# Kernel tuning notes

Hardware: AMD Instinct MI355X
Metric: run time of the kernel (lower is better)

## Reference

```python
import jax, jax.numpy as jnp
import numpy as np

N_NODES = 50000
N_EDGES = 800000
N_GRAPHS = 256
HIDDEN = 128
N_LAYERS = 5
OUT_DIM = 10
BN_EPS = 1e-5


def _batchnorm(z, gamma, beta):
    # training-mode BatchNorm1d over node axis, biased variance (as torch)
    m = z.mean(axis=0)
    v = z.var(axis=0)
    return (z - m) * jax.lax.rsqrt(v + BN_EPS) * gamma + beta


def setup_inputs() -> dict:
    key = jax.random.key(0)
    ks = jax.random.split(key, 16)
    s = 0.05
    x = jax.random.normal(ks[0], (N_NODES, HIDDEN), dtype=jnp.float32)
    edge_index = jax.random.randint(ks[1], (2, N_EDGES), 0, N_NODES, dtype=jnp.int32)
    batch = jnp.sort(jax.random.randint(ks[2], (N_NODES,), 0, N_GRAPHS, dtype=jnp.int32))
    return {
        "x": x,
        "conv_W1": jax.random.normal(ks[3], (N_LAYERS, HIDDEN, HIDDEN), dtype=jnp.float32) * s,
        "conv_b1": jnp.zeros((N_LAYERS, HIDDEN), jnp.float32),
        "mlp_bn_g": jnp.ones((N_LAYERS, HIDDEN), jnp.float32),
        "mlp_bn_b": jnp.zeros((N_LAYERS, HIDDEN), jnp.float32),
        "conv_W2": jax.random.normal(ks[4], (N_LAYERS, HIDDEN, HIDDEN), dtype=jnp.float32) * s,
        "conv_b2": jnp.zeros((N_LAYERS, HIDDEN), jnp.float32),
        "out_bn_g": jnp.ones((N_LAYERS, HIDDEN), jnp.float32),
        "out_bn_b": jnp.zeros((N_LAYERS, HIDDEN), jnp.float32),
        "fc1_W": jax.random.normal(ks[5], (HIDDEN * N_LAYERS, HIDDEN), dtype=jnp.float32) * s,
        "fc1_b": jnp.zeros((HIDDEN,), jnp.float32),
        "fc2_W": jax.random.normal(ks[6], (HIDDEN, OUT_DIM), dtype=jnp.float32) * s,
        "fc2_b": jnp.zeros((OUT_DIM,), jnp.float32),
        "edge_index": edge_index,
        "batch": batch,
    }


def reference(x, conv_W1, conv_b1, mlp_bn_g, mlp_bn_b, conv_W2, conv_b2,
              out_bn_g, out_bn_b, fc1_W, fc1_b, fc2_W, fc2_b,
              edge_index, batch):
    src, dst = edge_index[0], edge_index[1]
    h = x
    pooled = []
    for i in range(N_LAYERS):
        # GINConv, eps=0: mlp(h + sum_{j in N(v)} h_j)
        agg = jax.ops.segment_sum(h[src], dst, num_segments=N_NODES)
        z = h + agg
        z = z @ conv_W1[i] + conv_b1[i]
        z = jax.nn.relu(_batchnorm(z, mlp_bn_g[i], mlp_bn_b[i]))
        z = z @ conv_W2[i] + conv_b2[i]
        # outer BN + ReLU (self.bns)
        h = jax.nn.relu(_batchnorm(z, out_bn_g[i], out_bn_b[i]))
        pooled.append(jax.ops.segment_sum(h, batch, num_segments=N_GRAPHS))
    out = jnp.concatenate(pooled, axis=-1)          # [G, L*hidden]
    out = jax.nn.relu(out @ fc1_W + fc1_b)
    # dropout in eval mode -> identity
    out = out @ fc2_W + fc2_b                       # [G, out_dim]
    return out
```

## Files before the change

### kernel.cpp

```cpp
#include <hip/hip_runtime.h>

#define N_NODES 50000
#define N_EDGES 800000
#define N_GRAPHS 256
#define HIDDEN 128
#define N_LAYERS 5
#define OUT_DIM 10
#define BN_EPS 1e-5f

#define BUCKET_SHIFT 7
#define BUCKET_NODES 128
#define N_BUCKETS ((N_NODES + BUCKET_NODES - 1) / BUCKET_NODES)
#define STAGE_THREADS 1024
#define STAGE_EPB 4096

typedef __bf16 bf16x8 __attribute__((ext_vector_type(8)));
typedef float f32x4 __attribute__((ext_vector_type(4)));

union FragAB {
    bf16x8 v;
    ushort s[8];
    uint4 q;
};

__device__ inline float bf2f(ushort u) {
    union { uint i; float f; } v;
    v.i = ((uint)u) << 16;
    return v.f;
}

__device__ inline float bf2f_lo(uint u) {
    union { uint i; float f; } v;
    v.i = u << 16;
    return v.f;
}

__device__ inline float bf2f_hi(uint u) {
    union { uint i; float f; } v;
    v.i = u & 0xffff0000u;
    return v.f;
}

__device__ inline ushort f2bf(float f) {
    union { float f; uint u; } v;
    v.f = f;
    uint b = v.u;
    uint r = (b + 0x7fffu + ((b >> 16) & 1u)) >> 16;
    return (ushort)r;
}


__global__ void k_hist(const int* __restrict__ dst, int* __restrict__ counts) {
    int e = blockIdx.x * blockDim.x + threadIdx.x;
    if (e < N_EDGES) atomicAdd(&counts[dst[e]], 1);
}

__global__ void k_scan_blocks(const int* __restrict__ in, int* __restrict__ out,
                              int* __restrict__ bsum, int n) {
    __shared__ int s[256];
    int i = blockIdx.x * 256 + threadIdx.x;
    int v = (i < n) ? in[i] : 0;
    s[threadIdx.x] = v;
    __syncthreads();
    for (int off = 1; off < 256; off <<= 1) {
        int t = (threadIdx.x >= off) ? s[threadIdx.x - off] : 0;
        __syncthreads();
        s[threadIdx.x] += t;
        __syncthreads();
    }
    if (i < n) out[i] = s[threadIdx.x];
    if (threadIdx.x == 255) bsum[blockIdx.x] = s[255];
}

__global__ void k_scan_sums(int* __restrict__ bsum, int nb) {
    __shared__ int s[256];
    int t = threadIdx.x;
    int v = (t < nb) ? bsum[t] : 0;
    s[t] = v;
    __syncthreads();
    for (int off = 1; off < 256; off <<= 1) {
        int tv = (t >= off) ? s[t - off] : 0;
        __syncthreads();
        s[t] += tv;
        __syncthreads();
    }
    int excl = (t == 0) ? 0 : s[t - 1];
    if (t < nb) bsum[t] = excl;
}

__global__ void k_offsets(const int* __restrict__ scanned, const int* __restrict__ boff,
                          int* __restrict__ offsets, int* __restrict__ bcur, int n) {
    int i = blockIdx.x * 256 + threadIdx.x;
    if (i < n) {
        int val = scanned[i] + boff[blockIdx.x];
        offsets[i + 1] = val;
        if (((i + 1) & (BUCKET_NODES - 1)) == 0 && (i + 1) < n)
            bcur[(i + 1) >> BUCKET_SHIFT] = val;
    }
    if (i == 0) {
        offsets[0] = 0;
        bcur[0] = 0;
    }
}

__global__ __launch_bounds__(STAGE_THREADS) void k_stage(const int* __restrict__ esrc,
                                                         const int* __restrict__ edst,
                                                         int* __restrict__ bcur,
                                                         uint* __restrict__ stage) {
    __shared__ int lcnt[N_BUCKETS];
    __shared__ int lbase[N_BUCKETS];
    int tid = threadIdx.x;
    for (int i = tid; i < N_BUCKETS; i += STAGE_THREADS) lcnt[i] = 0;
    __syncthreads();
    int e0 = blockIdx.x * STAGE_EPB;
    uint pk[4];
    int bk[4];
    bool val[4];
#pragma unroll
    for (int i = 0; i < 4; ++i) {
        int e = e0 + i * STAGE_THREADS + tid;
        val[i] = e < N_EDGES;
        bk[i] = 0;
        pk[i] = 0;
        if (val[i]) {
            int d = edst[e];
            int s = esrc[e];
            bk[i] = d >> BUCKET_SHIFT;
            pk[i] = (uint)s | ((uint)(d & (BUCKET_NODES - 1)) << 16);
            atomicAdd(&lcnt[bk[i]], 1);
        }
    }
    __syncthreads();
    for (int i = tid; i < N_BUCKETS; i += STAGE_THREADS) {
        int c = lcnt[i];
        lbase[i] = c ? atomicAdd(&bcur[i], c) : 0;
        lcnt[i] = 0;
    }
    __syncthreads();
#pragma unroll
    for (int i = 0; i < 4; ++i) {
        if (val[i]) {
            int off = atomicAdd(&lcnt[bk[i]], 1);
            stage[lbase[bk[i]] + off] = pk[i];
        }
    }
}

__global__ __launch_bounds__(256) void k_fill2(const uint* __restrict__ stage,
                                               const int* __restrict__ offsets,
                                               ushort* __restrict__ adj) {
    __shared__ int lcur[BUCKET_NODES];
    int bk = blockIdx.x;
    int n0 = bk * BUCKET_NODES;
    int n1 = n0 + BUCKET_NODES;
    if (n1 > N_NODES) n1 = N_NODES;
    int cnt = n1 - n0;
    if ((int)threadIdx.x < cnt) lcur[threadIdx.x] = offsets[n0 + threadIdx.x];
    __syncthreads();
    int s = offsets[n0];
    int e = offsets[n1];
    for (int i = s + threadIdx.x; i < e; i += 256) {
        uint pk = stage[i];
        int dl = pk >> 16;
        int pos = atomicAdd(&lcur[dl], 1);
        adj[pos] = (ushort)(pk & 0xffffu);
    }
}


#define CVT_BLKS 6250

__global__ __launch_bounds__(256) void k_prep(const float* __restrict__ x,
                                              ushort* __restrict__ xb,
                                              const float* __restrict__ W1,
                                              const float* __restrict__ W2,
                                              ushort* __restrict__ Wp) {
    if (blockIdx.x < CVT_BLKS) {
        int i = blockIdx.x * 256 + threadIdx.x;
        float4 v = ((const float4*)x)[i];
        ushort4 o;
        o.x = f2bf(v.x); o.y = f2bf(v.y); o.z = f2bf(v.z); o.w = f2bf(v.w);
        ((ushort4*)xb)[i] = o;
    } else {
        int mat = blockIdx.x - CVT_BLKS;
        const float* src = (mat < 5) ? (W1 + (size_t)mat * 16384)
                                     : (W2 + (size_t)(mat - 5) * 16384);
        ushort* dst = Wp + (size_t)mat * 16384;
        for (int idx = threadIdx.x; idx < 16384; idx += 256) {
            int jj = idx & 7;
            int frag = idx >> 3;
            int lane = frag & 63;
            int cf = frag >> 6;
            int ct = cf >> 2, kc = cf & 3;
            int k = kc * 32 + (lane >> 4) * 8 + jj;
            int c = (lane & 15) * 8 + ct;
            dst[idx] = f2bf(src[k * 128 + c]);
        }
    }
}


__global__ __launch_bounds__(256) void k_agg(const ushort* __restrict__ h,
                                             const int* __restrict__ offsets,
                                             const ushort* __restrict__ adj,
                                             ushort* __restrict__ y) {
    int wave = threadIdx.x >> 6;
    int lane = threadIdx.x & 63;
    int e = lane >> 4, c16 = lane & 15;
    int v = blockIdx.x * 4 + wave;
    const uint4* h4 = (const uint4*)h;

    int off = offsets[v];
    int end = offsets[v + 1];

    float a0 = 0.f, a1 = 0.f, a2 = 0.f, a3 = 0.f;
    float a4 = 0.f, a5 = 0.f, a6 = 0.f, a7 = 0.f;

#define ACC8(T)                                      \
    {                                                \
        a0 += bf2f_lo(T.x); a1 += bf2f_hi(T.x);      \
        a2 += bf2f_lo(T.y); a3 += bf2f_hi(T.y);      \
        a4 += bf2f_lo(T.z); a5 += bf2f_hi(T.z);      \
        a6 += bf2f_lo(T.w); a7 += bf2f_hi(T.w);      \
    }

    int u[8];
    bool val[8];
#pragma unroll
    for (int k = 0; k < 8; ++k) {
        int idx = off + k * 4 + e;
        val[k] = idx < end;
        u[k] = adj[val[k] ? idx : 0];
    }
    uint4 t[8];
#pragma unroll
    for (int k = 0; k < 8; ++k)
        t[k] = h4[(size_t)u[k] * 16 + c16];
#pragma unroll
    for (int k = 0; k < 8; ++k) {
        if (val[k]) ACC8(t[k])
    }

    for (int j = off + 32; j < end; j += 4) {
        bool valid = (j + e) < end;
        int uu = adj[valid ? (j + e) : 0];
        uint4 tt = h4[(size_t)uu * 16 + c16];
        if (valid) ACC8(tt)
    }

    a0 += __shfl_xor(a0, 16, 64); a0 += __shfl_xor(a0, 32, 64);
    a1 += __shfl_xor(a1, 16, 64); a1 += __shfl_xor(a1, 32, 64);
    a2 += __shfl_xor(a2, 16, 64); a2 += __shfl_xor(a2, 32, 64);
    a3 += __shfl_xor(a3, 16, 64); a3 += __shfl_xor(a3, 32, 64);
    a4 += __shfl_xor(a4, 16, 64); a4 += __shfl_xor(a4, 32, 64);
    a5 += __shfl_xor(a5, 16, 64); a5 += __shfl_xor(a5, 32, 64);
    a6 += __shfl_xor(a6, 16, 64); a6 += __shfl_xor(a6, 32, 64);
    a7 += __shfl_xor(a7, 16, 64); a7 += __shfl_xor(a7, 32, 64);
    if (e == 0) {
        uint4 self = h4[(size_t)v * 16 + c16];
        ACC8(self)
        uint4 pk;
        pk.x = (uint)f2bf(a0) | ((uint)f2bf(a1) << 16);
        pk.y = (uint)f2bf(a2) | ((uint)f2bf(a3) << 16);
        pk.z = (uint)f2bf(a4) | ((uint)f2bf(a5) << 16);
        pk.w = (uint)f2bf(a6) | ((uint)f2bf(a7) << 16);
        ((uint4*)y)[(size_t)v * 16 + c16] = pk;
    }
#undef ACC8
}


template <bool ACT>
__global__ __launch_bounds__(256) void k_gemm(const ushort* __restrict__ A,
                                              const ushort* __restrict__ Wp,
                                              const float* __restrict__ bias,
                                              const float* __restrict__ g,
                                              const float* __restrict__ b,
                                              const float* __restrict__ statIn,
                                              ushort* __restrict__ Z,
                                              float* __restrict__ statOut) {
    __shared__ float scs[128];
    __shared__ float shs[128];
    __shared__ float redS[4][128];
    __shared__ float redQ[4][128];

    int tid = threadIdx.x;
    int w = tid >> 6, lane = tid & 63;
    int m = lane & 15, quad = lane >> 4;
    int r0 = blockIdx.x * 64;

    if (ACT) {
        if (tid < 128) {
            float s = 0.f, q = 0.f;
#pragma unroll
            for (int sl = 0; sl < 8; ++sl) {
                s += statIn[sl * 256 + tid];
                q += statIn[sl * 256 + 128 + tid];
            }
            float mn = s * (1.f / N_NODES);
            float var = q * (1.f / N_NODES) - mn * mn;
            float sc = g[tid] * rsqrtf(var + BN_EPS);
            scs[tid] = sc;
            shs[tid] = b[tid] - mn * sc;
        }
        __syncthreads();
    }

    int arow = r0 + w * 16 + m;
    if (arow >= N_NODES) arow = N_NODES - 1;

    f32x4 acc[8];
#pragma unroll
    for (int ct = 0; ct < 8; ++ct) acc[ct] = (f32x4){0.f, 0.f, 0.f, 0.f};

    const uint4* Wp4 = (const uint4*)Wp;

#pragma unroll
    for (int kc = 0; kc < 4; ++kc) {
        FragAB a;
        a.q = *(const uint4*)(A + (size_t)arow * 128 + kc * 32 + quad * 8);
        if (ACT) {
            int k0 = kc * 32 + quad * 8;
#pragma unroll
            for (int jj = 0; jj < 8; ++jj) {
                float fv = bf2f(a.s[jj]);
                fv = fmaxf(fv * scs[k0 + jj] + shs[k0 + jj], 0.f);
                a.s[jj] = f2bf(fv);
            }
        }
#pragma unroll
        for (int ct = 0; ct < 8; ++ct) {
            FragAB bf;
            bf.q = Wp4[(ct * 4 + kc) * 64 + lane];
            acc[ct] = __builtin_amdgcn_mfma_f32_16x16x32_bf16(a.v, bf.v, acc[ct], 0, 0, 0);
        }
    }

    int rbase = r0 + w * 16 + quad * 4;
    float bc[8];
#pragma unroll
    for (int ct = 0; ct < 8; ++ct) bc[ct] = bias[m * 8 + ct];

    float st[8], sq[8];
#pragma unroll
    for (int ct = 0; ct < 8; ++ct) { st[ct] = 0.f; sq[ct] = 0.f; }

#pragma unroll
    for (int i = 0; i < 4; ++i) {
        int row = rbase + i;
        if (row < N_NODES) {
            float v[8];
#pragma unroll
            for (int ct = 0; ct < 8; ++ct) {
                v[ct] = acc[ct][i] + bc[ct];
                st[ct] += v[ct];
                sq[ct] += v[ct] * v[ct];
            }
            uint4 pk;
            pk.x = (uint)f2bf(v[0]) | ((uint)f2bf(v[1]) << 16);
            pk.y = (uint)f2bf(v[2]) | ((uint)f2bf(v[3]) << 16);
            pk.z = (uint)f2bf(v[4]) | ((uint)f2bf(v[5]) << 16);
            pk.w = (uint)f2bf(v[6]) | ((uint)f2bf(v[7]) << 16);
            *(uint4*)(Z + (size_t)row * 128 + m * 8) = pk;
        }
    }
#pragma unroll
    for (int ct = 0; ct < 8; ++ct) {
        st[ct] += __shfl_xor(st[ct], 16, 64);
        st[ct] += __shfl_xor(st[ct], 32, 64);
        sq[ct] += __shfl_xor(sq[ct], 16, 64);
        sq[ct] += __shfl_xor(sq[ct], 32, 64);
    }
    if (quad == 0) {
#pragma unroll
        for (int ct = 0; ct < 8; ++ct) {
            redS[w][m * 8 + ct] = st[ct];
            redQ[w][m * 8 + ct] = sq[ct];
        }
    }
    __syncthreads();
    if (tid < 128) {
        float s = redS[0][tid] + redS[1][tid] + redS[2][tid] + redS[3][tid];
        float q = redQ[0][tid] + redQ[1][tid] + redQ[2][tid] + redQ[3][tid];
        int slot = (blockIdx.x & 7) * 256;
        atomicAdd(&statOut[slot + tid], s);
        atomicAdd(&statOut[slot + 128 + tid], q);
    }
}


__global__ __launch_bounds__(256) void k_apply_pool(const ushort* __restrict__ z2,
                                                    const float* __restrict__ statIn,
                                                    const float* __restrict__ g,
                                                    const float* __restrict__ b,
                                                    const int* __restrict__ batch,
                                                    ushort* __restrict__ h,
                                                    float* __restrict__ pooled) {
    int w = threadIdx.x >> 6, lane = threadIdx.x & 63;
    int c0 = lane * 2;
    float s0 = 0.f, q0 = 0.f, s1 = 0.f, q1 = 0.f;
#pragma unroll
    for (int sl = 0; sl < 8; ++sl) {
        s0 += statIn[sl * 256 + c0];
        q0 += statIn[sl * 256 + 128 + c0];
        s1 += statIn[sl * 256 + c0 + 1];
        q1 += statIn[sl * 256 + 128 + c0 + 1];
    }
    float mn0 = s0 * (1.f / N_NODES);
    float var0 = q0 * (1.f / N_NODES) - mn0 * mn0;
    float sc0 = g[c0] * rsqrtf(var0 + BN_EPS);
    float sh0 = b[c0] - mn0 * sc0;
    float mn1 = s1 * (1.f / N_NODES);
    float var1 = q1 * (1.f / N_NODES) - mn1 * mn1;
    float sc1 = g[c0 + 1] * rsqrtf(var1 + BN_EPS);
    float sh1 = b[c0 + 1] - mn1 * sc1;

    int r0 = blockIdx.x * 256 + w * 64;
    int r1 = r0 + 64;
    if (r1 > N_NODES) r1 = N_NODES;
    if (r0 >= N_NODES) return;

    int bidx = r0 + lane;
    int myb = batch[bidx < N_NODES ? bidx : (N_NODES - 1)];

    float a0 = 0.f, a1 = 0.f;
    int curg = -1;
    const uint* z1 = (const uint*)z2;
    uint* h1 = (uint*)h;
    for (int r = r0; r < r1; ++r) {
        uint t = z1[(size_t)r * 64 + lane];
        float v0 = fmaxf(bf2f((ushort)(t & 0xffff)) * sc0 + sh0, 0.f);
        float v1 = fmaxf(bf2f((ushort)(t >> 16)) * sc1 + sh1, 0.f);
        h1[(size_t)r * 64 + lane] = (uint)f2bf(v0) | ((uint)f2bf(v1) << 16);
        int gg = __shfl(myb, r - r0, 64);
        if (gg != curg) {
            if (curg >= 0) {
                atomicAdd(&pooled[(size_t)curg * 640 + c0], a0);
                atomicAdd(&pooled[(size_t)curg * 640 + c0 + 1], a1);
            }
            a0 = 0.f; a1 = 0.f;
            curg = gg;
        }
        a0 += v0;
        a1 += v1;
    }
    if (curg >= 0) {
        atomicAdd(&pooled[(size_t)curg * 640 + c0], a0);
        atomicAdd(&pooled[(size_t)curg * 640 + c0 + 1], a1);
    }
}


__global__ __launch_bounds__(128) void k_mlp(const float* __restrict__ pooled,
                                             const float* __restrict__ fc1W,
                                             const float* __restrict__ fc1b,
                                             const float* __restrict__ fc2W,
                                             const float* __restrict__ fc2b,
                                             float* __restrict__ out) {
    __shared__ float p[640];
    __shared__ float hid[128];
    int g = blockIdx.x;
    int t = threadIdx.x;
    for (int i = t; i < 640; i += 128) p[i] = pooled[(size_t)g * 640 + i];
    __syncthreads();
    float a = fc1b[t];
    for (int k = 0; k < 640; ++k) a += p[k] * fc1W[(size_t)k * 128 + t];
    hid[t] = fmaxf(a, 0.f);
    __syncthreads();
    if (t < OUT_DIM) {
        float o = fc2b[t];
#pragma unroll 8
        for (int c = 0; c < 128; ++c) o += hid[c] * fc2W[(size_t)c * OUT_DIM + t];
        out[(size_t)g * OUT_DIM + t] = o;
    }
}


static inline char* align256(char* p) {
    return (char*)(((uintptr_t)p + 255) & ~(uintptr_t)255);
}

extern "C" void kernel_launch(void* const* d_in, const int* in_sizes, int n_in,
                              void* d_out, int out_size, void* d_ws, size_t ws_size,
                              hipStream_t stream) {
    const float* x    = (const float*)d_in[0];
    const float* W1   = (const float*)d_in[1];
    const float* b1   = (const float*)d_in[2];
    const float* bng1 = (const float*)d_in[3];
    const float* bnb1 = (const float*)d_in[4];
    const float* W2   = (const float*)d_in[5];
    const float* b2   = (const float*)d_in[6];
    const float* bng2 = (const float*)d_in[7];
    const float* bnb2 = (const float*)d_in[8];
    const float* fc1W = (const float*)d_in[9];
    const float* fc1b = (const float*)d_in[10];
    const float* fc2W = (const float*)d_in[11];
    const float* fc2b = (const float*)d_in[12];
    const int* ei     = (const int*)d_in[13];
    const int* batch  = (const int*)d_in[14];
    const int* esrc = ei;
    const int* edst = ei + N_EDGES;

    const size_t NF = (size_t)N_NODES * HIDDEN;
    char* p = (char*)d_ws;
    ushort* ybf  = (ushort*)p; p = align256(p + NF * 2);
    ushort* z1bf = (ushort*)p; p = align256(p + NF * 2);
    ushort* hbf  = (ushort*)p; p = align256(p + NF * 2);
    ushort* xbf  = (ushort*)p; p = align256(p + NF * 2);
    ushort* Wp   = (ushort*)p; p = align256(p + (size_t)10 * 16384 * 2);
    float* pooled = (float*)p; p += (size_t)N_GRAPHS * 640 * 4;
    float* stats  = (float*)p; p = align256(p + (size_t)10 * 8 * 256 * 4);
    int* counts   = (int*)p; p = align256(p + (size_t)N_NODES * 4);
    int* offsets  = (int*)p; p = align256(p + (size_t)(N_NODES + 1) * 4);
    int* bcur     = (int*)p; p = align256(p + (size_t)N_BUCKETS * 4);
    int* bsum     = (int*)p; p = align256(p + 256 * 4);
    ushort* adj   = (ushort*)p; p = align256(p + (size_t)N_EDGES * 2);
    uint* stage   = (uint*)p; p = align256(p + (size_t)N_EDGES * 4);

    hipMemsetAsync(counts, 0, (size_t)N_NODES * 4, stream);
    hipMemsetAsync(pooled, 0, ((size_t)N_GRAPHS * 640 + (size_t)10 * 8 * 256) * 4, stream);

    const int SCAN_BLKS = (N_NODES + 255) / 256;
    k_hist<<<(N_EDGES + 255) / 256, 256, 0, stream>>>(edst, counts);
    {
        int* scanscratch = (int*)stage;
        k_scan_blocks<<<SCAN_BLKS, 256, 0, stream>>>(counts, scanscratch, bsum, N_NODES);
        k_scan_sums<<<1, 256, 0, stream>>>(bsum, SCAN_BLKS);
        k_offsets<<<SCAN_BLKS, 256, 0, stream>>>(scanscratch, bsum, offsets, bcur, N_NODES);
    }
    k_stage<<<(N_EDGES + STAGE_EPB - 1) / STAGE_EPB, STAGE_THREADS, 0, stream>>>(esrc, edst, bcur, stage);
    k_fill2<<<N_BUCKETS, 256, 0, stream>>>(stage, offsets, adj);

    k_prep<<<CVT_BLKS + 10, 256, 0, stream>>>(x, xbf, W1, W2, Wp);

    const int GEMM_BLKS = (N_NODES + 63) / 64;
    const int POOL_BLKS = (N_NODES + 255) / 256;
    for (int l = 0; l < N_LAYERS; ++l) {
        const ushort* hin = (l == 0) ? xbf : hbf;
        float* st1 = stats + (size_t)(2 * l) * 2048;
        float* st2 = stats + (size_t)(2 * l + 1) * 2048;

        k_agg<<<N_NODES / 4, 256, 0, stream>>>(hin, offsets, adj, ybf);

        k_gemm<false><<<GEMM_BLKS, 256, 0, stream>>>(
            ybf, Wp + (size_t)l * 16384, b1 + l * 128,
            nullptr, nullptr, nullptr, z1bf, st1);

        k_gemm<true><<<GEMM_BLKS, 256, 0, stream>>>(
            z1bf, Wp + (size_t)(5 + l) * 16384, b2 + l * 128,
            bng1 + l * 128, bnb1 + l * 128, st1, ybf, st2);

        k_apply_pool<<<POOL_BLKS, 256, 0, stream>>>(
            ybf, st2, bng2 + l * 128, bnb2 + l * 128, batch, hbf, pooled + l * 128);
    }

    k_mlp<<<N_GRAPHS, 128, 0, stream>>>(pooled, fc1W, fc1b, fc2W, fc2b, (float*)d_out);
}
```

Baseline: 568.3 us.

## Fuse outer BN+ReLU into next layer's aggregation and merge pooling launch

Drops the materialized h tensor. The outer BatchNorm+ReLU is now applied on the fly to z2 inside the next layer's neighbor gather, and that kernel also runs the graph pooling in separate blocks of the same launch. This removes a full write of h per layer and one kernel launch per layer. In exchange the BN affine+ReLU is recomputed for every gathered edge (about 16x per node), adding ALU work to the gather path and some register pressure.

```diff
diff --git a/kernel.cpp b/kernel.cpp
--- a/kernel.cpp
+++ b/kernel.cpp
@@ -13,6 +13,8 @@
 #define N_BUCKETS ((N_NODES + BUCKET_NODES - 1) / BUCKET_NODES)
 #define STAGE_THREADS 1024
 #define STAGE_EPB 4096
+#define POOL_BLKS ((N_NODES + 255) / 256)
+#define AGG_BLKS (N_NODES / 4)
 
 typedef __bf16 bf16x8 __attribute__((ext_vector_type(8)));
 typedef float f32x4 __attribute__((ext_vector_type(4)));
@@ -200,29 +202,38 @@
 }
 
 
-__global__ __launch_bounds__(256) void k_agg(const ushort* __restrict__ h,
-                                             const int* __restrict__ offsets,
-                                             const ushort* __restrict__ adj,
-                                             ushort* __restrict__ y) {
-    int wave = threadIdx.x >> 6;
-    int lane = threadIdx.x & 63;
-    int e = lane >> 4, c16 = lane & 15;
-    int v = blockIdx.x * 4 + wave;
-    const uint4* h4 = (const uint4*)h;
-
+#define ACC8_BN(T)                                                  \
+    {                                                               \
+        float f0 = bf2f_lo(T.x), f1 = bf2f_hi(T.x);                 \
+        float f2 = bf2f_lo(T.y), f3 = bf2f_hi(T.y);                 \
+        float f4 = bf2f_lo(T.z), f5 = bf2f_hi(T.z);                 \
+        float f6 = bf2f_lo(T.w), f7 = bf2f_hi(T.w);                 \
+        if (BN) {                                                   \
+            f0 = fmaxf(f0 * sc[0] + sh[0], 0.f);                    \
+            f1 = fmaxf(f1 * sc[1] + sh[1], 0.f);                    \
+            f2 = fmaxf(f2 * sc[2] + sh[2], 0.f);                    \
+            f3 = fmaxf(f3 * sc[3] + sh[3], 0.f);                    \
+            f4 = fmaxf(f4 * sc[4] + sh[4], 0.f);                    \
+            f5 = fmaxf(f5 * sc[5] + sh[5], 0.f);                    \
+            f6 = fmaxf(f6 * sc[6] + sh[6], 0.f);                    \
+            f7 = fmaxf(f7 * sc[7] + sh[7], 0.f);                    \
+        }                                                           \
+        a0 += f0; a1 += f1; a2 += f2; a3 += f3;                     \
+        a4 += f4; a5 += f5; a6 += f6; a7 += f7;                     \
+    }
+
+template <bool BN>
+__device__ inline void agg_one_node(int v, const uint4* __restrict__ h4,
+                                    const int* __restrict__ offsets,
+                                    const ushort* __restrict__ adj,
+                                    ushort* __restrict__ y,
+                                    int e, int c16,
+                                    const float* sc, const float* sh) {
     int off = offsets[v];
     int end = offsets[v + 1];
 
     float a0 = 0.f, a1 = 0.f, a2 = 0.f, a3 = 0.f;
     float a4 = 0.f, a5 = 0.f, a6 = 0.f, a7 = 0.f;
-
-#define ACC8(T)                                      \
-    {                                                \
-        a0 += bf2f_lo(T.x); a1 += bf2f_hi(T.x);      \
-        a2 += bf2f_lo(T.y); a3 += bf2f_hi(T.y);      \
-        a4 += bf2f_lo(T.z); a5 += bf2f_hi(T.z);      \
-        a6 += bf2f_lo(T.w); a7 += bf2f_hi(T.w);      \
-    }
 
     int u[8];
     bool val[8];
@@ -238,14 +249,13 @@
         t[k] = h4[(size_t)u[k] * 16 + c16];
 #pragma unroll
     for (int k = 0; k < 8; ++k) {
-        if (val[k]) ACC8(t[k])
-    }
-
+        if (val[k]) ACC8_BN(t[k])
+    }
     for (int j = off + 32; j < end; j += 4) {
         bool valid = (j + e) < end;
         int uu = adj[valid ? (j + e) : 0];
         uint4 tt = h4[(size_t)uu * 16 + c16];
-        if (valid) ACC8(tt)
+        if (valid) ACC8_BN(tt)
     }
 
     a0 += __shfl_xor(a0, 16, 64); a0 += __shfl_xor(a0, 32, 64);
@@ -258,7 +268,7 @@
     a7 += __shfl_xor(a7, 16, 64); a7 += __shfl_xor(a7, 32, 64);
     if (e == 0) {
         uint4 self = h4[(size_t)v * 16 + c16];
-        ACC8(self)
+        ACC8_BN(self)
         uint4 pk;
         pk.x = (uint)f2bf(a0) | ((uint)f2bf(a1) << 16);
         pk.y = (uint)f2bf(a2) | ((uint)f2bf(a3) << 16);
@@ -266,7 +276,168 @@
         pk.w = (uint)f2bf(a6) | ((uint)f2bf(a7) << 16);
         ((uint4*)y)[(size_t)v * 16 + c16] = pk;
     }
-#undef ACC8
+}
+
+__global__ __launch_bounds__(256) void k_agg_first(const ushort* __restrict__ h,
+                                                   const int* __restrict__ offsets,
+                                                   const ushort* __restrict__ adj,
+                                                   ushort* __restrict__ y) {
+    int wave = threadIdx.x >> 6;
+    int lane = threadIdx.x & 63;
+    int v = blockIdx.x * 4 + wave;
+    agg_one_node<false>(v, (const uint4*)h, offsets, adj, y,
+                        lane >> 4, lane & 15, nullptr, nullptr);
+}
+
+__global__ __launch_bounds__(256) void k_aggpool(const ushort* __restrict__ z2,
+                                                 const float* __restrict__ statIn,
+                                                 const float* __restrict__ g,
+                                                 const float* __restrict__ b,
+                                                 const int* __restrict__ batch,
+                                                 float* __restrict__ pooled,
+                                                 const int* __restrict__ offsets,
+                                                 const ushort* __restrict__ adj,
+                                                 ushort* __restrict__ y) {
+    int tid = threadIdx.x;
+    int w = tid >> 6, lane = tid & 63;
+
+    if (blockIdx.x >= POOL_BLKS) {
+        __shared__ float scs[128];
+        __shared__ float shs[128];
+        if (tid < 128) {
+            float s = 0.f, q = 0.f;
+#pragma unroll
+            for (int sl = 0; sl < 8; ++sl) {
+                s += statIn[sl * 256 + tid];
+                q += statIn[sl * 256 + 128 + tid];
+            }
+            float mn = s * (1.f / N_NODES);
+            float var = q * (1.f / N_NODES) - mn * mn;
+            float scv = g[tid] * rsqrtf(var + BN_EPS);
+            scs[tid] = scv;
+            shs[tid] = b[tid] - mn * scv;
+        }
+        __syncthreads();
+        int c16 = lane & 15;
+        float sc[8], sh[8];
+#pragma unroll
+        for (int j = 0; j < 8; ++j) {
+            sc[j] = scs[c16 * 8 + j];
+            sh[j] = shs[c16 * 8 + j];
+        }
+        int v = (blockIdx.x - POOL_BLKS) * 4 + w;
+        agg_one_node<true>(v, (const uint4*)z2, offsets, adj, y,
+                           lane >> 4, c16, sc, sh);
+        return;
+    }
+
+    int c0 = lane * 2;
+    float s0 = 0.f, q0 = 0.f, s1 = 0.f, q1 = 0.f;
+#pragma unroll
+    for (int sl = 0; sl < 8; ++sl) {
+        s0 += statIn[sl * 256 + c0];
+        q0 += statIn[sl * 256 + 128 + c0];
+        s1 += statIn[sl * 256 + c0 + 1];
+        q1 += statIn[sl * 256 + 128 + c0 + 1];
+    }
+    float mn0 = s0 * (1.f / N_NODES);
+    float var0 = q0 * (1.f / N_NODES) - mn0 * mn0;
+    float sc0 = g[c0] * rsqrtf(var0 + BN_EPS);
+    float sh0 = b[c0] - mn0 * sc0;
+    float mn1 = s1 * (1.f / N_NODES);
+    float var1 = q1 * (1.f / N_NODES) - mn1 * mn1;
+    float sc1 = g[c0 + 1] * rsqrtf(var1 + BN_EPS);
+    float sh1 = b[c0 + 1] - mn1 * sc1;
+
+    int r0 = blockIdx.x * 256 + w * 64;
+    int r1 = r0 + 64;
+    if (r1 > N_NODES) r1 = N_NODES;
+    if (r0 >= N_NODES) return;
+
+    int bidx = r0 + lane;
+    int myb = batch[bidx < N_NODES ? bidx : (N_NODES - 1)];
+
+    float a0 = 0.f, a1 = 0.f;
+    int curg = -1;
+    const uint* z1 = (const uint*)z2;
+    for (int r = r0; r < r1; ++r) {
+        uint t = z1[(size_t)r * 64 + lane];
+        float v0 = fmaxf(bf2f((ushort)(t & 0xffff)) * sc0 + sh0, 0.f);
+        float v1 = fmaxf(bf2f((ushort)(t >> 16)) * sc1 + sh1, 0.f);
+        int gg = __shfl(myb, r - r0, 64);
+        if (gg != curg) {
+            if (curg >= 0) {
+                atomicAdd(&pooled[(size_t)curg * 640 + c0], a0);
+                atomicAdd(&pooled[(size_t)curg * 640 + c0 + 1], a1);
+            }
+            a0 = 0.f; a1 = 0.f;
+            curg = gg;
+        }
+        a0 += v0;
+        a1 += v1;
+    }
+    if (curg >= 0) {
+        atomicAdd(&pooled[(size_t)curg * 640 + c0], a0);
+        atomicAdd(&pooled[(size_t)curg * 640 + c0 + 1], a1);
+    }
+}
+
+__global__ __launch_bounds__(256) void k_pool(const ushort* __restrict__ z2,
+                                              const float* __restrict__ statIn,
+                                              const float* __restrict__ g,
+                                              const float* __restrict__ b,
+                                              const int* __restrict__ batch,
+                                              float* __restrict__ pooled) {
+    int w = threadIdx.x >> 6, lane = threadIdx.x & 63;
+    int c0 = lane * 2;
+    float s0 = 0.f, q0 = 0.f, s1 = 0.f, q1 = 0.f;
+#pragma unroll
+    for (int sl = 0; sl < 8; ++sl) {
+        s0 += statIn[sl * 256 + c0];
+        q0 += statIn[sl * 256 + 128 + c0];
+        s1 += statIn[sl * 256 + c0 + 1];
+        q1 += statIn[sl * 256 + 128 + c0 + 1];
+    }
+    float mn0 = s0 * (1.f / N_NODES);
+    float var0 = q0 * (1.f / N_NODES) - mn0 * mn0;
+    float sc0 = g[c0] * rsqrtf(var0 + BN_EPS);
+    float sh0 = b[c0] - mn0 * sc0;
+    float mn1 = s1 * (1.f / N_NODES);
+    float var1 = q1 * (1.f / N_NODES) - mn1 * mn1;
+    float sc1 = g[c0 + 1] * rsqrtf(var1 + BN_EPS);
+    float sh1 = b[c0 + 1] - mn1 * sc1;
+
+    int r0 = blockIdx.x * 256 + w * 64;
+    int r1 = r0 + 64;
+    if (r1 > N_NODES) r1 = N_NODES;
+    if (r0 >= N_NODES) return;
+
+    int bidx = r0 + lane;
+    int myb = batch[bidx < N_NODES ? bidx : (N_NODES - 1)];
+
+    float a0 = 0.f, a1 = 0.f;
+    int curg = -1;
+    const uint* z1 = (const uint*)z2;
+    for (int r = r0; r < r1; ++r) {
+        uint t = z1[(size_t)r * 64 + lane];
+        float v0 = fmaxf(bf2f((ushort)(t & 0xffff)) * sc0 + sh0, 0.f);
+        float v1 = fmaxf(bf2f((ushort)(t >> 16)) * sc1 + sh1, 0.f);
+        int gg = __shfl(myb, r - r0, 64);
+        if (gg != curg) {
+            if (curg >= 0) {
+                atomicAdd(&pooled[(size_t)curg * 640 + c0], a0);
+                atomicAdd(&pooled[(size_t)curg * 640 + c0 + 1], a1);
+            }
+            a0 = 0.f; a1 = 0.f;
+            curg = gg;
+        }
+        a0 += v0;
+        a1 += v1;
+    }
+    if (curg >= 0) {
+        atomicAdd(&pooled[(size_t)curg * 640 + c0], a0);
+        atomicAdd(&pooled[(size_t)curg * 640 + c0 + 1], a1);
+    }
 }
 
 
@@ -385,68 +556,6 @@
         int slot = (blockIdx.x & 7) * 256;
         atomicAdd(&statOut[slot + tid], s);
         atomicAdd(&statOut[slot + 128 + tid], q);
-    }
-}
-
-
-__global__ __launch_bounds__(256) void k_apply_pool(const ushort* __restrict__ z2,
-                                                    const float* __restrict__ statIn,
-                                                    const float* __restrict__ g,
-                                                    const float* __restrict__ b,
-                                                    const int* __restrict__ batch,
-                                                    ushort* __restrict__ h,
-                                                    float* __restrict__ pooled) {
-    int w = threadIdx.x >> 6, lane = threadIdx.x & 63;
-    int c0 = lane * 2;
-    float s0 = 0.f, q0 = 0.f, s1 = 0.f, q1 = 0.f;
-#pragma unroll
-    for (int sl = 0; sl < 8; ++sl) {
-        s0 += statIn[sl * 256 + c0];
-        q0 += statIn[sl * 256 + 128 + c0];
-        s1 += statIn[sl * 256 + c0 + 1];
-        q1 += statIn[sl * 256 + 128 + c0 + 1];
-    }
-    float mn0 = s0 * (1.f / N_NODES);
-    float var0 = q0 * (1.f / N_NODES) - mn0 * mn0;
-    float sc0 = g[c0] * rsqrtf(var0 + BN_EPS);
-    float sh0 = b[c0] - mn0 * sc0;
-    float mn1 = s1 * (1.f / N_NODES);
-    float var1 = q1 * (1.f / N_NODES) - mn1 * mn1;
-    float sc1 = g[c0 + 1] * rsqrtf(var1 + BN_EPS);
-    float sh1 = b[c0 + 1] - mn1 * sc1;
-
-    int r0 = blockIdx.x * 256 + w * 64;
-    int r1 = r0 + 64;
-    if (r1 > N_NODES) r1 = N_NODES;
-    if (r0 >= N_NODES) return;
-
-    int bidx = r0 + lane;
-    int myb = batch[bidx < N_NODES ? bidx : (N_NODES - 1)];
-
-    float a0 = 0.f, a1 = 0.f;
-    int curg = -1;
-    const uint* z1 = (const uint*)z2;
-    uint* h1 = (uint*)h;
-    for (int r = r0; r < r1; ++r) {
-        uint t = z1[(size_t)r * 64 + lane];
-        float v0 = fmaxf(bf2f((ushort)(t & 0xffff)) * sc0 + sh0, 0.f);
-        float v1 = fmaxf(bf2f((ushort)(t >> 16)) * sc1 + sh1, 0.f);
-        h1[(size_t)r * 64 + lane] = (uint)f2bf(v0) | ((uint)f2bf(v1) << 16);
-        int gg = __shfl(myb, r - r0, 64);
-        if (gg != curg) {
-            if (curg >= 0) {
-                atomicAdd(&pooled[(size_t)curg * 640 + c0], a0);
-                atomicAdd(&pooled[(size_t)curg * 640 + c0 + 1], a1);
-            }
-            a0 = 0.f; a1 = 0.f;
-            curg = gg;
-        }
-        a0 += v0;
-        a1 += v1;
-    }
-    if (curg >= 0) {
-        atomicAdd(&pooled[(size_t)curg * 640 + c0], a0);
-        atomicAdd(&pooled[(size_t)curg * 640 + c0 + 1], a1);
     }
 }
 
@@ -505,7 +614,7 @@
     char* p = (char*)d_ws;
     ushort* ybf  = (ushort*)p; p = align256(p + NF * 2);
     ushort* z1bf = (ushort*)p; p = align256(p + NF * 2);
-    ushort* hbf  = (ushort*)p; p = align256(p + NF * 2);
+    ushort* z2bf = (ushort*)p; p = align256(p + NF * 2);
     ushort* xbf  = (ushort*)p; p = align256(p + NF * 2);
     ushort* Wp   = (ushort*)p; p = align256(p + (size_t)10 * 16384 * 2);
     float* pooled = (float*)p; p += (size_t)N_GRAPHS * 640 * 4;
@@ -534,13 +643,18 @@
     k_prep<<<CVT_BLKS + 10, 256, 0, stream>>>(x, xbf, W1, W2, Wp);
 
     const int GEMM_BLKS = (N_NODES + 63) / 64;
-    const int POOL_BLKS = (N_NODES + 255) / 256;
     for (int l = 0; l < N_LAYERS; ++l) {
-        const ushort* hin = (l == 0) ? xbf : hbf;
         float* st1 = stats + (size_t)(2 * l) * 2048;
         float* st2 = stats + (size_t)(2 * l + 1) * 2048;
 
-        k_agg<<<N_NODES / 4, 256, 0, stream>>>(hin, offsets, adj, ybf);
+        if (l == 0) {
+            k_agg_first<<<AGG_BLKS, 256, 0, stream>>>(xbf, offsets, adj, ybf);
+        } else {
+            float* st2prev = stats + (size_t)(2 * l - 1) * 2048;
+            k_aggpool<<<POOL_BLKS + AGG_BLKS, 256, 0, stream>>>(
+                z2bf, st2prev, bng2 + (l - 1) * 128, bnb2 + (l - 1) * 128,
+                batch, pooled + (l - 1) * 128, offsets, adj, ybf);
+        }
 
         k_gemm<false><<<GEMM_BLKS, 256, 0, stream>>>(
             ybf, Wp + (size_t)l * 16384, b1 + l * 128,
@@ -548,11 +662,13 @@
 
         k_gemm<true><<<GEMM_BLKS, 256, 0, stream>>>(
             z1bf, Wp + (size_t)(5 + l) * 16384, b2 + l * 128,
-            bng1 + l * 128, bnb1 + l * 128, st1, ybf, st2);
-
-        k_apply_pool<<<POOL_BLKS, 256, 0, stream>>>(
-            ybf, st2, bng2 + l * 128, bnb2 + l * 128, batch, hbf, pooled + l * 128);
-    }
+            bng1 + l * 128, bnb1 + l * 128, st1, z2bf, st2);
+    }
+
+    k_pool<<<POOL_BLKS, 256, 0, stream>>>(
+        z2bf, stats + (size_t)(2 * N_LAYERS - 1) * 2048,
+        bng2 + (N_LAYERS - 1) * 128, bnb2 + (N_LAYERS - 1) * 128,
+        batch, pooled + (N_LAYERS - 1) * 128);
 
     k_mlp<<<N_GRAPHS, 128, 0, stream>>>(pooled, fc1W, fc1b, fc2W, fc2b, (float*)d_out);
 }
```

After: 514.3 us. 1.11x faster.
